# Performance work log

Hardware: AMD Instinct MI355X
Metric: run time of the kernel (lower is better)

Reference implementation:

```python
import jax, jax.numpy as jnp
import numpy as np

EMBED_DIM = 1024
ATTN_DIM = 1024
BATCH = 4
SEQ = 2048


def setup_inputs() -> dict:
    key = jax.random.key(0)
    k1, k2, k3, k4 = jax.random.split(key, 4)
    embedded = jax.random.normal(k1, (BATCH, SEQ, EMBED_DIM), dtype=jnp.float32)
    # torch Linear weights have shape [out_features, in_features]
    scale = 1.0 / np.sqrt(EMBED_DIM)
    W_K = jax.random.uniform(k2, (ATTN_DIM, EMBED_DIM), dtype=jnp.float32, minval=-scale, maxval=scale)
    W_Q = jax.random.uniform(k3, (ATTN_DIM, EMBED_DIM), dtype=jnp.float32, minval=-scale, maxval=scale)
    W_V = jax.random.uniform(k4, (ATTN_DIM, EMBED_DIM), dtype=jnp.float32, minval=-scale, maxval=scale)
    return {"embedded": embedded, "W_K": W_K, "W_Q": W_Q, "W_V": W_V}


def reference(embedded, W_K, W_Q, W_V):
    # embedded: [B, L, E]; W_*: [A, E] (torch Linear layout, applied as x @ W.T)
    L = embedded.shape[1]
    A = W_K.shape[0]
    K = jnp.einsum('ble,ae->bla', embedded, W_K)
    Q = jnp.einsum('ble,ae->bla', embedded, W_Q)
    V = jnp.einsum('ble,ae->bla', embedded, W_V)
    att = jnp.einsum('bqa,bka->bqk', Q, K) / jnp.sqrt(jnp.float32(A))  # [B, L, L]
    causal = jnp.tril(jnp.ones((L, L), dtype=bool))  # lower-triangular mask
    att = jnp.where(causal, att, -jnp.inf)
    att = jax.nn.softmax(att, axis=-1)
    return jnp.einsum('bqk,bka->bqa', att, V)
```

## Files before the change

kernel.cpp:

```cpp
#include <hip/hip_runtime.h>
#include <hip/hip_bf16.h>
#include <stdint.h>

#define BATCH 4
#define SEQ   2048
#define EMB   1024
#define ADIM  1024

typedef __attribute__((ext_vector_type(8))) short  short8;
typedef __attribute__((ext_vector_type(4))) float  float4v;

static __device__ __forceinline__ unsigned short f2bf(float f) {
    unsigned int u = __float_as_uint(f);
    u += 0x7FFFu + ((u >> 16) & 1u);
    return (unsigned short)(u >> 16);
}

static __device__ __forceinline__ uint2 pack4(float4v v) {
    uint2 r;
    r.x = (unsigned)f2bf(v.x) | ((unsigned)f2bf(v.y) << 16);
    r.y = (unsigned)f2bf(v.z) | ((unsigned)f2bf(v.w) << 16);
    return r;
}

static __device__ __forceinline__ void gload16(const void* g, void* l) {
    __builtin_amdgcn_global_load_lds(
        (const __attribute__((address_space(1))) void*)g,
        (__attribute__((address_space(3))) void*)l, 16, 0, 0);
}

__global__ __launch_bounds__(256) void prep_kernel(
    const float* __restrict__ X,  const float* __restrict__ Wv,
    const float* __restrict__ Wq, const float* __restrict__ Wk,
    unsigned short* __restrict__ Xb, unsigned short* __restrict__ Wvb,
    unsigned short* __restrict__ WqT, unsigned short* __restrict__ WkT,
    float* __restrict__ rowsum, float* __restrict__ out)
{
    __shared__ unsigned short T[64][72];
    const int bI = blockIdx.x;
    if (bI < 4608) {
        const float* src; unsigned short* dst; int off;
        if (bI < 4096) { src = X;  dst = Xb;  off = bI; }
        else           { src = Wv; dst = Wvb; off = bI - 4096; }
        const int i = (off * 256 + threadIdx.x) * 8;
        float4v a = *(const float4v*)(src + i);
        float4v b = *(const float4v*)(src + i + 4);
        uint2 pa = pack4(a), pb = pack4(b);
        uint4 o; o.x = pa.x; o.y = pa.y; o.z = pb.x; o.w = pb.y;
        *(uint4*)(dst + i) = o;
        return;
    }
    if (bI < 4616) {
        const int i = ((bI - 4608) * 256 + threadIdx.x) * 4;
        *(float4v*)(rowsum + i) = float4v{0.f, 0.f, 0.f, 0.f};
        return;
    }
    if (bI >= 5128) {
        const int o   = bI - 5128;
        const int b   = o >> 10;
        const int blk = o & 1023;
        float* dst = out + ((size_t)(b * 2048 + 1024) * 1024)
                         + (size_t)blk * 1024 + threadIdx.x * 4;
        *(float4v*)dst = float4v{0.f, 0.f, 0.f, 0.f};
        return;
    }
    const int z    = (bI - 4616) >> 8;
    const int tile = (bI - 4616) & 255;
    const int ti = tile >> 4;
    const int tj = tile & 15;
    const float* W = z ? Wk : Wq;
    unsigned short* WT = z ? WkT : WqT;
    const int t  = threadIdx.x;
    const int r  = t >> 2;
    const int c  = (t & 3) << 4;

    const float* src = W + (size_t)(ti * 64 + r) * EMB + tj * 64 + c;
    #pragma unroll
    for (int u = 0; u < 4; ++u) {
        float4v v = *(const float4v*)(src + 4 * u);
        uint2 p = pack4(v);
        *(uint2*)&T[r][c + 4 * u] = p;
    }
    __syncthreads();
    unsigned short tmp[16];
    #pragma unroll
    for (int u = 0; u < 16; ++u) tmp[u] = T[c + u][r];
    unsigned short* dst = WT + (size_t)(tj * 64 + r) * EMB + ti * 64 + c;
    *(uint4*)(dst)     = *(uint4*)&tmp[0];
    *(uint4*)(dst + 8) = *(uint4*)&tmp[8];
}

static __device__ __forceinline__ void gemm_core(
    const unsigned short* __restrict__ A, const unsigned short* __restrict__ B,
    int lda, int ldb, int m0, int n0, int klen,
    unsigned short* As, unsigned short* Bs, float4v acc[4][4])
{
    const int tid  = threadIdx.x;
    const int r    = tid >> 2;
    const int c8   = (tid & 3) << 3;
    const int lane = tid & 63;
    const int wave = tid >> 6;
    const int quad = lane >> 4;
    const int l16  = lane & 15;
    const int wm   = (wave >> 1) << 6;
    const int wn   = (wave & 1) << 6;

    const unsigned short* Ag = A + (size_t)(m0 + r) * lda + c8;
    const unsigned short* Bg = B + (size_t)(n0 + r) * ldb + c8;
    unsigned short* Al = As + tid * 8;
    unsigned short* Bl = Bs + tid * 8;
    const int niter = klen >> 5;

    #define ISSUE(k0, st) do { \
        unsigned short* al_ = Al + (st) * 4096; \
        unsigned short* bl_ = Bl + (st) * 4096; \
        gload16(Ag + (k0),                    al_); \
        gload16(Ag + (k0) + (size_t)64 * lda, al_ + 2048); \
        gload16(Bg + (k0),                    bl_); \
        gload16(Bg + (k0) + (size_t)64 * ldb, bl_ + 2048); \
    } while (0)

    ISSUE(0, 0);
    ISSUE(32, 1);

    int ci = 0, ii = 2;
    for (int it = 0; it < niter; ++it) {
        const int knext = (it + 2 < niter) ? ((it + 2) << 5) : 0;
        ISSUE(knext, ii);
        asm volatile("s_waitcnt vmcnt(8)" ::: "memory");
        asm volatile("s_barrier" ::: "memory");

        const unsigned short* Ah = As + ci * 4096;
        const unsigned short* Bh = Bs + ci * 4096;
        short8 af[4], bfr[4];
        #pragma unroll
        for (int i = 0; i < 4; ++i)
            af[i] = *(const short8*)&Ah[(wm + 16 * i + l16) * 32 + quad * 8];
        #pragma unroll
        for (int j = 0; j < 4; ++j)
            bfr[j] = *(const short8*)&Bh[(wn + 16 * j + l16) * 32 + quad * 8];
        #pragma unroll
        for (int i = 0; i < 4; ++i)
            #pragma unroll
            for (int j = 0; j < 4; ++j)
                acc[i][j] = __builtin_amdgcn_mfma_f32_16x16x32_bf16(af[i], bfr[j], acc[i][j], 0, 0, 0);

        asm volatile("s_barrier" ::: "memory");
        ci = (ci == 2) ? 0 : ci + 1;
        ii = (ii == 2) ? 0 : ii + 1;
    }
    asm volatile("s_waitcnt vmcnt(0)" ::: "memory");
    #undef ISSUE
}

#define DECL_TILE_IDX() \
    const int lane = threadIdx.x & 63; \
    const int wave = threadIdx.x >> 6; \
    const int quad = lane >> 4; \
    const int l16  = lane & 15; \
    const int wm   = (wave >> 1) << 6; \
    const int wn   = (wave & 1) << 6;

__global__ __launch_bounds__(256, 3) void m_kernel(
    const unsigned short* __restrict__ WkT, const unsigned short* __restrict__ WqT,
    float* __restrict__ Mtf)
{
    __shared__ __align__(16) unsigned short As[3 * 128 * 32];
    __shared__ __align__(16) unsigned short Bs[3 * 128 * 32];
    const int idx = blockIdx.x;
    const int kc  = idx >> 6;
    const int t   = idx & 63;
    const int m0  = (t >> 3) << 7;
    const int n0  = (t & 7) << 7;

    float4v acc[4][4];
    #pragma unroll
    for (int i = 0; i < 4; ++i)
        #pragma unroll
        for (int j = 0; j < 4; ++j)
            acc[i][j] = float4v{0.f, 0.f, 0.f, 0.f};

    gemm_core(WkT + kc * 256, WqT + kc * 256, EMB, EMB, m0, n0, 256, As, Bs, acc);

    float* dst = Mtf + (size_t)kc * 1024 * 1024;
    DECL_TILE_IDX();
    #pragma unroll
    for (int i = 0; i < 4; ++i)
        #pragma unroll
        for (int j = 0; j < 4; ++j)
            #pragma unroll
            for (int rr = 0; rr < 4; ++rr) {
                const int row = m0 + wm + 16 * i + quad * 4 + rr;
                const int col = n0 + wn + 16 * j + l16;
                dst[(size_t)row * EMB + col] = acc[i][j][rr];
            }
}

__global__ __launch_bounds__(256) void mc_kernel(
    const float* __restrict__ Mtf, unsigned short* __restrict__ Mt)
{
    const int base = (blockIdx.x * 256 + threadIdx.x) * 16;
    #pragma unroll
    for (int u = 0; u < 4; ++u) {
        const int i = base + u * 4;
        float4v s = *(const float4v*)(Mtf + i);
        s = s + *(const float4v*)(Mtf + 1048576 + i);
        s = s + *(const float4v*)(Mtf + 2097152 + i);
        s = s + *(const float4v*)(Mtf + 3145728 + i);
        s = s * 0.03125f;
        uint2 p = pack4(s);
        *(uint2*)(Mt + i) = p;
    }
}

__global__ __launch_bounds__(256, 2) void qv_kernel(
    const unsigned short* __restrict__ Xb, const unsigned short* __restrict__ Mt,
    const unsigned short* __restrict__ Wvb,
    unsigned short* __restrict__ Qpb, unsigned short* __restrict__ Vtb)
{
    __shared__ __align__(16) unsigned short LDS[3 * 4096 + 3 * 8192];
    unsigned short* As = LDS;
    unsigned short* Bs = LDS + 3 * 4096;
    const int idx = blockIdx.x;
    const int x   = idx & 7;
    const int j   = idx >> 3;
    const int sl  = j & 7;
    const int g   = j >> 3;
    const int z   = sl >> 2;
    const int n0  = (sl & 3) << 8;
    const int b   = g & 3;
    const int qt  = (g >> 2) ? (15 - x) : x;
    const int m0  = (b * 16 + qt) << 7;
    const unsigned short* B = (z == 0) ? Mt : Wvb;

    const int tid  = threadIdx.x;
    const int r    = tid >> 2;
    const int c8   = (tid & 3) << 3;
    const int lane = tid & 63;
    const int wave = tid >> 6;
    const int quad = lane >> 4;
    const int l16  = lane & 15;
    const int wm   = (wave >> 1) << 6;
    const int wn   = (wave & 1) << 7;

    float4v acc[4][8];
    #pragma unroll
    for (int i = 0; i < 4; ++i)
        #pragma unroll
        for (int jj = 0; jj < 8; ++jj)
            acc[i][jj] = float4v{0.f, 0.f, 0.f, 0.f};

    const unsigned short* Ag = Xb + (size_t)(m0 + r) * EMB + c8;
    const unsigned short* Bg = B  + (size_t)(n0 + r) * EMB + c8;
    unsigned short* Al = As + tid * 8;
    unsigned short* Bl = Bs + tid * 8;

    #define ISSUE_W(k0, st) do { \
        unsigned short* al_ = Al + (st) * 4096; \
        unsigned short* bl_ = Bl + (st) * 8192; \
        gload16(Ag + (k0),                     al_); \
        gload16(Ag + (k0) + (size_t)64  * EMB, al_ + 2048); \
        gload16(Bg + (k0),                     bl_); \
        gload16(Bg + (k0) + (size_t)64  * EMB, bl_ + 2048); \
        gload16(Bg + (k0) + (size_t)128 * EMB, bl_ + 4096); \
        gload16(Bg + (k0) + (size_t)192 * EMB, bl_ + 6144); \
    } while (0)

    ISSUE_W(0, 0);
    ISSUE_W(32, 1);

    int ci = 0, ii = 2;
    for (int it = 0; it < 32; ++it) {
        const int knext = (it + 2 < 32) ? ((it + 2) << 5) : 0;
        ISSUE_W(knext, ii);
        asm volatile("s_waitcnt vmcnt(12)" ::: "memory");
        asm volatile("s_barrier" ::: "memory");

        const unsigned short* Ah = As + ci * 4096;
        const unsigned short* Bh = Bs + ci * 8192;
        short8 af[4], bfr[8];
        #pragma unroll
        for (int i = 0; i < 4; ++i)
            af[i] = *(const short8*)&Ah[(wm + 16 * i + l16) * 32 + quad * 8];
        #pragma unroll
        for (int jj = 0; jj < 8; ++jj)
            bfr[jj] = *(const short8*)&Bh[(wn + 16 * jj + l16) * 32 + quad * 8];
        #pragma unroll
        for (int i = 0; i < 4; ++i)
            #pragma unroll
            for (int jj = 0; jj < 8; ++jj)
                acc[i][jj] = __builtin_amdgcn_mfma_f32_16x16x32_bf16(af[i], bfr[jj], acc[i][jj], 0, 0, 0);

        asm volatile("s_barrier" ::: "memory");
        ci = (ci == 2) ? 0 : ci + 1;
        ii = (ii == 2) ? 0 : ii + 1;
    }
    asm volatile("s_waitcnt vmcnt(0)" ::: "memory");
    #undef ISSUE_W

    if (z == 0) {
        #pragma unroll
        for (int i = 0; i < 4; ++i)
            #pragma unroll
            for (int jj = 0; jj < 8; ++jj)
                #pragma unroll
                for (int rr = 0; rr < 4; ++rr) {
                    const int row = m0 + wm + 16 * i + quad * 4 + rr;
                    const int col = n0 + wn + 16 * jj + l16;
                    Qpb[(size_t)row * ADIM + col] = f2bf(acc[i][jj][rr]);
                }
    } else {
        __syncthreads();
        unsigned short* T = LDS;
        #pragma unroll
        for (int i = 0; i < 4; ++i)
            #pragma unroll
            for (int jj = 0; jj < 8; ++jj) {
                const int qrow = wm + 16 * i + quad * 4;
                const int acol = wn + 16 * jj + l16;
                uint2 w;
                w.x = (unsigned)f2bf(acc[i][jj][0]) | ((unsigned)f2bf(acc[i][jj][1]) << 16);
                w.y = (unsigned)f2bf(acc[i][jj][2]) | ((unsigned)f2bf(acc[i][jj][3]) << 16);
                *(uint2*)&T[acol * 136 + qrow] = w;
            }
        __syncthreads();
        const int bb = m0 >> 11;
        const int l0 = m0 & (SEQ - 1);
        unsigned short* dst = Vtb + (((size_t)(bb * ADIM + n0 + tid)) << 11) + l0;
        #pragma unroll
        for (int u = 0; u < 16; ++u)
            *(uint4*)(dst + u * 8) = *(const uint4*)&T[tid * 136 + u * 8];
    }
}

__global__ __launch_bounds__(256, 3) void s_kernel(
    const unsigned short* __restrict__ Qpb, const unsigned short* __restrict__ Xb,
    unsigned short* __restrict__ E, float* __restrict__ rowsum)
{
    const int idx = blockIdx.x;
    const int x   = idx & 7;
    const int j   = idx >> 3;
    const int b   = j / 17;
    const int u   = j - b * 17;
    const int qt  = (u <= x) ? x : 15 - x;
    const int kt  = (u <= x) ? u : u - (x + 1);
    const int q0  = qt << 7;
    const int k0  = kt << 7;

    __shared__ __align__(16) unsigned short As[3 * 128 * 32];
    __shared__ __align__(16) unsigned short Bs[3 * 128 * 32];

    float4v acc[4][4];
    #pragma unroll
    for (int i = 0; i < 4; ++i)
        #pragma unroll
        for (int jj = 0; jj < 4; ++jj)
            acc[i][jj] = float4v{0.f, 0.f, 0.f, 0.f};

    gemm_core(Qpb + (size_t)b * SEQ * ADIM, Xb + (size_t)b * SEQ * EMB,
              ADIM, EMB, q0, k0, EMB, As, Bs, acc);

    unsigned short* Eb = E + (size_t)b * SEQ * SEQ;
    float* rsb = rowsum + (size_t)b * SEQ;
    DECL_TILE_IDX();
    #pragma unroll
    for (int i = 0; i < 4; ++i)
        #pragma unroll
        for (int rr = 0; rr < 4; ++rr) {
            const int row = q0 + wm + 16 * i + quad * 4 + rr;
            float s = 0.f;
            #pragma unroll
            for (int jj = 0; jj < 4; ++jj) {
                const int col = k0 + wn + 16 * jj + l16;
                float e = (col <= row) ? __expf(acc[i][jj][rr]) : 0.f;
                s += e;
                Eb[(size_t)row * SEQ + col] = f2bf(e);
            }
            s += __shfl_xor(s, 1);
            s += __shfl_xor(s, 2);
            s += __shfl_xor(s, 4);
            s += __shfl_xor(s, 8);
            if (l16 == 0) atomicAdd(&rsb[row], s);
        }
}

__global__ __launch_bounds__(256, 3) void pv_kernel(
    const unsigned short* __restrict__ E, const unsigned short* __restrict__ Vtb,
    const float* __restrict__ rowsum, float* __restrict__ out)
{
    const int idx  = blockIdx.x;
    const int x    = idx & 7;
    const int j    = idx >> 3;
    const int slot = j >> 5;
    const int c    = j & 31;
    const int b    = c >> 3;
    const int a0   = (c & 7) << 7;

    int qt, kbeg, klen, dual;
    if (slot == 0)      { qt = x;      kbeg = 0;    klen = (x + 1) << 7; dual = 0; }
    else if (slot == 1) { qt = 15 - x; kbeg = 0;    klen = 1024;         dual = 1; }
    else                { qt = 15 - x; kbeg = 1024; klen = (8 - x) << 7; dual = 1; }
    const int q0 = qt << 7;

    __shared__ __align__(16) unsigned short As[3 * 128 * 32];
    __shared__ __align__(16) unsigned short Bs[3 * 128 * 32];

    float4v acc[4][4];
    #pragma unroll
    for (int i = 0; i < 4; ++i)
        #pragma unroll
        for (int jj = 0; jj < 4; ++jj)
            acc[i][jj] = float4v{0.f, 0.f, 0.f, 0.f};

    gemm_core(E + (size_t)b * SEQ * SEQ + kbeg, Vtb + (size_t)b * ADIM * SEQ + kbeg,
              SEQ, SEQ, q0, a0, klen, As, Bs, acc);

    float* ob = out + (size_t)b * SEQ * ADIM;
    const float* rsb = rowsum + (size_t)b * SEQ;
    DECL_TILE_IDX();
    if (!dual) {
        #pragma unroll
        for (int i = 0; i < 4; ++i)
            #pragma unroll
            for (int rr = 0; rr < 4; ++rr) {
                const int row = q0 + wm + 16 * i + quad * 4 + rr;
                const float inv = 1.0f / rsb[row];
                #pragma unroll
                for (int jj = 0; jj < 4; ++jj) {
                    const int col = a0 + wn + 16 * jj + l16;
                    ob[(size_t)row * ADIM + col] = acc[i][jj][rr] * inv;
                }
            }
    } else {
        #pragma unroll
        for (int i = 0; i < 4; ++i)
            #pragma unroll
            for (int rr = 0; rr < 4; ++rr) {
                const int row = q0 + wm + 16 * i + quad * 4 + rr;
                const float inv = 1.0f / rsb[row];
                #pragma unroll
                for (int jj = 0; jj < 4; ++jj) {
                    const int col = a0 + wn + 16 * jj + l16;
                    atomicAdd(&ob[(size_t)row * ADIM + col], acc[i][jj][rr] * inv);
                }
            }
    }
}

extern "C" void kernel_launch(void* const* d_in, const int* in_sizes, int n_in,
                              void* d_out, int out_size, void* d_ws, size_t ws_size,
                              hipStream_t stream)
{
    const float* X  = (const float*)d_in[0];
    const float* Wk = (const float*)d_in[1];
    const float* Wq = (const float*)d_in[2];
    const float* Wv = (const float*)d_in[3];
    float* out = (float*)d_out;

    const size_t MB = 1024 * 1024;
    char* ws = (char*)d_ws;
    unsigned short* Xb  = (unsigned short*)(ws);
    unsigned short* Wvb = (unsigned short*)(ws + 16 * MB);
    unsigned short* WqT = (unsigned short*)(ws + 18 * MB);
    unsigned short* WkT = (unsigned short*)(ws + 20 * MB);
    unsigned short* Mt  = (unsigned short*)(ws + 22 * MB);
    unsigned short* Qpb = (unsigned short*)(ws + 24 * MB);
    unsigned short* E   = (unsigned short*)(ws + 40 * MB);
    unsigned short* Vtb = (unsigned short*)(ws + 72 * MB);
    float*          rowsum = (float*)(ws + 88 * MB);
    float*          Mtf = (float*)(ws + 40 * MB);

    hipLaunchKernelGGL(prep_kernel, dim3(9224), dim3(256), 0, stream,
                       X, Wv, Wq, Wk, Xb, Wvb, WqT, WkT, rowsum, out);
    hipLaunchKernelGGL(m_kernel, dim3(256), dim3(256), 0, stream, WkT, WqT, Mtf);
    hipLaunchKernelGGL(mc_kernel, dim3(256), dim3(256), 0, stream, Mtf, Mt);
    hipLaunchKernelGGL(qv_kernel, dim3(512), dim3(256), 0, stream,
                       Xb, Mt, Wvb, Qpb, Vtb);
    hipLaunchKernelGGL(s_kernel, dim3(544), dim3(256), 0, stream, Qpb, Xb, E, rowsum);
    hipLaunchKernelGGL(pv_kernel, dim3(768), dim3(256), 0, stream, E, Vtb, rowsum, out);
}
```

Measured before the change: 230.0 us.

## Enlarge qv GEMM tile to 256x256 with 512 threads and swizzled LDS

Rewrites the Q/V projection kernel to use 256x256 output tiles computed by 8 waves, halving the grid and splitting each k-step into two phases that interleave A and B loads with MFMA work, with s_setprio raised around the MFMAs. An XOR swizzle is added to the LDS layout in both gemm_core and qv_kernel to cut bank conflicts on fragment reads. The aim is more operand reuse per LDS byte and less global traffic per FLOP. In exchange, fewer blocks (256) may underfill the GPU, accumulator register pressure rises, and the V transpose epilogue now runs in two passes.

```diff
diff --git a/kernel.cpp b/kernel.cpp
--- a/kernel.cpp
+++ b/kernel.cpp
@@ -28,6 +28,8 @@
         (const __attribute__((address_space(1))) void*)g,
         (__attribute__((address_space(3))) void*)l, 16, 0, 0);
 }
+
+static __device__ __forceinline__ int swz8(int row) { return ((row >> 1) & 3) << 3; }
 
 __global__ __launch_bounds__(256) void prep_kernel(
     const float* __restrict__ X,  const float* __restrict__ Wv,
@@ -97,7 +99,7 @@
 {
     const int tid  = threadIdx.x;
     const int r    = tid >> 2;
-    const int c8   = (tid & 3) << 3;
+    const int c8   = ((tid & 3) << 3) ^ swz8(tid >> 2);
     const int lane = tid & 63;
     const int wave = tid >> 6;
     const int quad = lane >> 4;
@@ -134,11 +136,15 @@
         const unsigned short* Bh = Bs + ci * 4096;
         short8 af[4], bfr[4];
         #pragma unroll
-        for (int i = 0; i < 4; ++i)
-            af[i] = *(const short8*)&Ah[(wm + 16 * i + l16) * 32 + quad * 8];
-        #pragma unroll
-        for (int j = 0; j < 4; ++j)
-            bfr[j] = *(const short8*)&Bh[(wn + 16 * j + l16) * 32 + quad * 8];
+        for (int i = 0; i < 4; ++i) {
+            const int row = wm + 16 * i + l16;
+            af[i] = *(const short8*)&Ah[row * 32 + ((quad * 8) ^ swz8(row))];
+        }
+        #pragma unroll
+        for (int j = 0; j < 4; ++j) {
+            const int row = wn + 16 * j + l16;
+            bfr[j] = *(const short8*)&Bh[row * 32 + ((quad * 8) ^ swz8(row))];
+        }
         #pragma unroll
         for (int i = 0; i < 4; ++i)
             #pragma unroll
@@ -213,123 +219,154 @@
     }
 }
 
-__global__ __launch_bounds__(256, 2) void qv_kernel(
+__global__ __launch_bounds__(512, 2) void qv_kernel(
     const unsigned short* __restrict__ Xb, const unsigned short* __restrict__ Mt,
     const unsigned short* __restrict__ Wvb,
     unsigned short* __restrict__ Qpb, unsigned short* __restrict__ Vtb)
 {
-    __shared__ __align__(16) unsigned short LDS[3 * 4096 + 3 * 8192];
+    __shared__ __align__(16) unsigned short LDS[49152];
     unsigned short* As = LDS;
-    unsigned short* Bs = LDS + 3 * 4096;
-    const int idx = blockIdx.x;
-    const int x   = idx & 7;
-    const int j   = idx >> 3;
-    const int sl  = j & 7;
-    const int g   = j >> 3;
-    const int z   = sl >> 2;
-    const int n0  = (sl & 3) << 8;
-    const int b   = g & 3;
-    const int qt  = (g >> 2) ? (15 - x) : x;
-    const int m0  = (b * 16 + qt) << 7;
-    const unsigned short* B = (z == 0) ? Mt : Wvb;
+    unsigned short* Bs = LDS + 24576;
+
+    const int idx  = blockIdx.x;
+    const int mt   = ((idx & 7) << 2) | ((idx >> 3) & 3);
+    const int slot = idx >> 5;
+    const int z    = slot >> 2;
+    const int n0   = (slot & 3) << 8;
+    const int m0   = mt << 8;
+    const unsigned short* B = z ? Wvb : Mt;
 
     const int tid  = threadIdx.x;
-    const int r    = tid >> 2;
-    const int c8   = (tid & 3) << 3;
     const int lane = tid & 63;
     const int wave = tid >> 6;
     const int quad = lane >> 4;
     const int l16  = lane & 15;
-    const int wm   = (wave >> 1) << 6;
-    const int wn   = (wave & 1) << 7;
-
-    float4v acc[4][8];
-    #pragma unroll
-    for (int i = 0; i < 4; ++i)
-        #pragma unroll
-        for (int jj = 0; jj < 8; ++jj)
-            acc[i][jj] = float4v{0.f, 0.f, 0.f, 0.f};
-
-    const unsigned short* Ag = Xb + (size_t)(m0 + r) * EMB + c8;
-    const unsigned short* Bg = B  + (size_t)(n0 + r) * EMB + c8;
+    const int wm   = (wave >> 2) << 7;
+    const int wn   = (wave & 3) << 6;
+
+    const int srow = tid >> 2;
+    const int c8   = ((tid & 3) << 3) ^ swz8(srow);
+
+    const unsigned short* Ag0 = Xb + (size_t)(m0 + srow) * EMB + c8;
+    const unsigned short* Ag1 = Ag0 + (size_t)128 * EMB;
+    const unsigned short* Bg0 = B  + (size_t)(n0 + srow) * EMB + c8;
+    const unsigned short* Bg1 = Bg0 + (size_t)128 * EMB;
     unsigned short* Al = As + tid * 8;
     unsigned short* Bl = Bs + tid * 8;
 
-    #define ISSUE_W(k0, st) do { \
-        unsigned short* al_ = Al + (st) * 4096; \
-        unsigned short* bl_ = Bl + (st) * 8192; \
-        gload16(Ag + (k0),                     al_); \
-        gload16(Ag + (k0) + (size_t)64  * EMB, al_ + 2048); \
-        gload16(Bg + (k0),                     bl_); \
-        gload16(Bg + (k0) + (size_t)64  * EMB, bl_ + 2048); \
-        gload16(Bg + (k0) + (size_t)128 * EMB, bl_ + 4096); \
-        gload16(Bg + (k0) + (size_t)192 * EMB, bl_ + 6144); \
+    #define ISSUE_QA(t, st) do { \
+        gload16(Ag0 + (t) * 32, Al + (st) * 8192); \
+        gload16(Ag1 + (t) * 32, Al + (st) * 8192 + 4096); \
     } while (0)
-
-    ISSUE_W(0, 0);
-    ISSUE_W(32, 1);
+    #define ISSUE_QB(t, st) do { \
+        gload16(Bg0 + (t) * 32, Bl + (st) * 8192); \
+        gload16(Bg1 + (t) * 32, Bl + (st) * 8192 + 4096); \
+    } while (0)
+
+    float4v acc[8][4];
+    #pragma unroll
+    for (int i = 0; i < 8; ++i)
+        #pragma unroll
+        for (int j = 0; j < 4; ++j)
+            acc[i][j] = float4v{0.f, 0.f, 0.f, 0.f};
+
+    ISSUE_QA(0, 0); ISSUE_QB(0, 0);
+    ISSUE_QA(1, 1); ISSUE_QB(1, 1);
 
     int ci = 0, ii = 2;
     for (int it = 0; it < 32; ++it) {
-        const int knext = (it + 2 < 32) ? ((it + 2) << 5) : 0;
-        ISSUE_W(knext, ii);
-        asm volatile("s_waitcnt vmcnt(12)" ::: "memory");
+        const unsigned short* Ah = As + ci * 8192;
+        const unsigned short* Bh = Bs + ci * 8192;
+        short8 bfr[4];
+
+        if (it + 2 < 32) ISSUE_QA(it + 2, ii);
+        asm volatile("s_waitcnt vmcnt(6)" ::: "memory");
         asm volatile("s_barrier" ::: "memory");
-
-        const unsigned short* Ah = As + ci * 4096;
-        const unsigned short* Bh = Bs + ci * 8192;
-        short8 af[4], bfr[8];
-        #pragma unroll
-        for (int i = 0; i < 4; ++i)
-            af[i] = *(const short8*)&Ah[(wm + 16 * i + l16) * 32 + quad * 8];
-        #pragma unroll
-        for (int jj = 0; jj < 8; ++jj)
-            bfr[jj] = *(const short8*)&Bh[(wn + 16 * jj + l16) * 32 + quad * 8];
-        #pragma unroll
-        for (int i = 0; i < 4; ++i)
-            #pragma unroll
-            for (int jj = 0; jj < 8; ++jj)
-                acc[i][jj] = __builtin_amdgcn_mfma_f32_16x16x32_bf16(af[i], bfr[jj], acc[i][jj], 0, 0, 0);
-
+        {
+            short8 af[4];
+            #pragma unroll
+            for (int i = 0; i < 4; ++i) {
+                const int row = wm + 16 * i + l16;
+                af[i] = *(const short8*)&Ah[row * 32 + ((quad * 8) ^ swz8(row))];
+            }
+            #pragma unroll
+            for (int j = 0; j < 4; ++j) {
+                const int row = wn + 16 * j + l16;
+                bfr[j] = *(const short8*)&Bh[row * 32 + ((quad * 8) ^ swz8(row))];
+            }
+            __builtin_amdgcn_s_setprio(1);
+            #pragma unroll
+            for (int i = 0; i < 4; ++i)
+                #pragma unroll
+                for (int j = 0; j < 4; ++j)
+                    acc[i][j] = __builtin_amdgcn_mfma_f32_16x16x32_bf16(af[i], bfr[j], acc[i][j], 0, 0, 0);
+            __builtin_amdgcn_s_setprio(0);
+        }
+        asm volatile("s_barrier" ::: "memory");
+
+        if (it + 2 < 32) ISSUE_QB(it + 2, ii);
+        {
+            short8 af[4];
+            #pragma unroll
+            for (int i = 0; i < 4; ++i) {
+                const int row = wm + 64 + 16 * i + l16;
+                af[i] = *(const short8*)&Ah[row * 32 + ((quad * 8) ^ swz8(row))];
+            }
+            __builtin_amdgcn_s_setprio(1);
+            #pragma unroll
+            for (int i = 0; i < 4; ++i)
+                #pragma unroll
+                for (int j = 0; j < 4; ++j)
+                    acc[i + 4][j] = __builtin_amdgcn_mfma_f32_16x16x32_bf16(af[i], bfr[j], acc[i + 4][j], 0, 0, 0);
+            __builtin_amdgcn_s_setprio(0);
+        }
         asm volatile("s_barrier" ::: "memory");
         ci = (ci == 2) ? 0 : ci + 1;
         ii = (ii == 2) ? 0 : ii + 1;
     }
     asm volatile("s_waitcnt vmcnt(0)" ::: "memory");
-    #undef ISSUE_W
+    #undef ISSUE_QA
+    #undef ISSUE_QB
 
     if (z == 0) {
         #pragma unroll
-        for (int i = 0; i < 4; ++i)
-            #pragma unroll
-            for (int jj = 0; jj < 8; ++jj)
+        for (int i = 0; i < 8; ++i)
+            #pragma unroll
+            for (int j = 0; j < 4; ++j)
                 #pragma unroll
                 for (int rr = 0; rr < 4; ++rr) {
-                    const int row = m0 + wm + 16 * i + quad * 4 + rr;
-                    const int col = n0 + wn + 16 * jj + l16;
-                    Qpb[(size_t)row * ADIM + col] = f2bf(acc[i][jj][rr]);
+                    const int row = m0 + wm + ((i & 3) << 4) + ((i >> 2) << 6) + quad * 4 + rr;
+                    const int col = n0 + wn + 16 * j + l16;
+                    Qpb[(size_t)row * ADIM + col] = f2bf(acc[i][j][rr]);
                 }
     } else {
-        __syncthreads();
-        unsigned short* T = LDS;
-        #pragma unroll
-        for (int i = 0; i < 4; ++i)
-            #pragma unroll
-            for (int jj = 0; jj < 8; ++jj) {
-                const int qrow = wm + 16 * i + quad * 4;
-                const int acol = wn + 16 * jj + l16;
-                uint2 w;
-                w.x = (unsigned)f2bf(acc[i][jj][0]) | ((unsigned)f2bf(acc[i][jj][1]) << 16);
-                w.y = (unsigned)f2bf(acc[i][jj][2]) | ((unsigned)f2bf(acc[i][jj][3]) << 16);
-                *(uint2*)&T[acol * 136 + qrow] = w;
-            }
-        __syncthreads();
         const int bb = m0 >> 11;
         const int l0 = m0 & (SEQ - 1);
-        unsigned short* dst = Vtb + (((size_t)(bb * ADIM + n0 + tid)) << 11) + l0;
-        #pragma unroll
-        for (int u = 0; u < 16; ++u)
-            *(uint4*)(dst + u * 8) = *(const uint4*)&T[tid * 136 + u * 8];
+        #pragma unroll
+        for (int h = 0; h < 2; ++h) {
+            __syncthreads();
+            if ((wm >> 7) == h) {
+                #pragma unroll
+                for (int i = 0; i < 8; ++i)
+                    #pragma unroll
+                    for (int j = 0; j < 4; ++j) {
+                        const int qloc = ((i & 3) << 4) + ((i >> 2) << 6) + quad * 4;
+                        const int acol = wn + 16 * j + l16;
+                        uint2 w;
+                        w.x = (unsigned)f2bf(acc[i][j][0]) | ((unsigned)f2bf(acc[i][j][1]) << 16);
+                        w.y = (unsigned)f2bf(acc[i][j][2]) | ((unsigned)f2bf(acc[i][j][3]) << 16);
+                        *(uint2*)&LDS[acol * 136 + qloc] = w;
+                    }
+            }
+            __syncthreads();
+            const int acol = tid >> 1;
+            const int qh   = (tid & 1) << 6;
+            unsigned short* dst = Vtb + (((size_t)(bb * ADIM + n0 + acol)) << 11)
+                                      + l0 + h * 128 + qh;
+            #pragma unroll
+            for (int u = 0; u < 8; ++u)
+                *(uint4*)(dst + u * 8) = *(const uint4*)&LDS[acol * 136 + qh + u * 8];
+        }
     }
 }
 
@@ -474,7 +511,7 @@
                        X, Wv, Wq, Wk, Xb, Wvb, WqT, WkT, rowsum, out);
     hipLaunchKernelGGL(m_kernel, dim3(256), dim3(256), 0, stream, WkT, WqT, Mtf);
     hipLaunchKernelGGL(mc_kernel, dim3(256), dim3(256), 0, stream, Mtf, Mt);
-    hipLaunchKernelGGL(qv_kernel, dim3(512), dim3(256), 0, stream,
+    hipLaunchKernelGGL(qv_kernel, dim3(256), dim3(512), 0, stream,
                        Xb, Mt, Wvb, Qpb, Vtb);
     hipLaunchKernelGGL(s_kernel, dim3(544), dim3(256), 0, stream, Qpb, Xb, E, rowsum);
     hipLaunchKernelGGL(pv_kernel, dim3(768), dim3(256), 0, stream, E, Vtb, rowsum, out);
```

Measured after the change: 231.5 us. About the same (+0.6%).
